# Optimization experiments

Hardware: AMD Instinct MI355X
Metric: run time of the kernel (lower is better)

Reference implementation:

```python
import jax, jax.numpy as jnp
import numpy as np

N_NODES = 100000
N_EDGES = 1600000
F_IN = 256
HID = 256
N_CLS = 16
NUM_PROP = 3


def setup_inputs() -> dict:
    key = jax.random.key(0)
    ks = jax.random.split(key, 8)
    x = jax.random.normal(ks[0], (N_NODES, F_IN), dtype=jnp.float32)
    edge_index = jax.random.randint(ks[1], (2, N_EDGES), 0, N_NODES, dtype=jnp.int64)
    # Glorot-ish scaled weights
    W1 = jax.random.normal(ks[2], (F_IN, HID), dtype=jnp.float32) / np.sqrt(F_IN)
    b1 = jnp.zeros((HID,), dtype=jnp.float32)
    Wi = jax.random.normal(ks[3], (HID, HID), dtype=jnp.float32) / np.sqrt(HID)
    bi = jnp.zeros((HID,), dtype=jnp.float32)
    W2 = jax.random.normal(ks[4], (HID, N_CLS), dtype=jnp.float32) / np.sqrt(HID)
    b2 = jnp.zeros((N_CLS,), dtype=jnp.float32)
    return {"x": x, "edge_index": edge_index, "W1": W1, "b1": b1,
            "Wi": Wi, "bi": bi, "W2": W2, "b2": b2}


def _gcn_graph(edge_index, n_nodes, dtype):
    # PyG GCNConv default: add self-loops, symmetric normalization.
    loop = jnp.arange(n_nodes, dtype=edge_index.dtype)
    src = jnp.concatenate([edge_index[0], loop])  # message source (x_j)
    dst = jnp.concatenate([edge_index[1], loop])  # aggregation target
    deg = jax.ops.segment_sum(jnp.ones_like(dst, dtype=dtype), dst, num_segments=n_nodes)
    dis = jnp.where(deg > 0, jax.lax.rsqrt(jnp.maximum(deg, 1.0)), 0.0)
    norm = dis[src] * dis[dst]  # [E+N]
    return src, dst, norm


def _gcn_conv(h, W, b, src, dst, norm, n_nodes):
    h = h @ W                                   # [N, out]
    msg = h[src] * norm[:, None]                # gather + scale, [E+N, out]
    out = jax.ops.segment_sum(msg, dst, num_segments=n_nodes)
    return out + b


def reference(x, edge_index, W1, b1, Wi, bi, W2, b2):
    n = x.shape[0]
    src, dst, norm = _gcn_graph(edge_index, n, x.dtype)
    h = _gcn_conv(x, W1, b1, src, dst, norm, n)
    # dropout p=0.25 is identity in eval mode (training=False)
    for _ in range(NUM_PROP):
        h = _gcn_conv(h, Wi, bi, src, dst, norm, n)
    h = jax.nn.relu(h)
    h = _gcn_conv(h, W2, b2, src, dst, norm, n)
    return jax.nn.softmax(h, axis=0)  # Softmax(dim=0): over nodes
```

## Files before the change

### kernel.cpp

```cpp
#include <hip/hip_runtime.h>
#include <cstdint>
#include <cstddef>

#define NFEAT 256
#define NCLS  16

typedef unsigned int uint;
typedef unsigned short ushort;
typedef __attribute__((ext_vector_type(8))) short short8;
typedef __attribute__((ext_vector_type(4))) float f32x4;

__device__ inline float blo(uint u) { return __uint_as_float(u << 16); }
__device__ inline float bhi(uint u) { return __uint_as_float(u & 0xffff0000u); }
__device__ inline ushort f2bf(float f) {
    uint b = __float_as_uint(f);
    b += 0x7fffu + ((b >> 16) & 1u);
    return (ushort)(b >> 16);
}
__device__ inline uint pack2(float a, float b) {
    return (uint)f2bf(a) | ((uint)f2bf(b) << 16);
}

__global__ void k_count(const int* __restrict__ dst, int* __restrict__ counts, int E) {
    int i = blockIdx.x * 256 + threadIdx.x;
    if (i < E) atomicAdd(&counts[dst[i]], 1);
}

__global__ void k_dis(const int* __restrict__ counts, float* __restrict__ dis, int Nn) {
    int i = blockIdx.x * 256 + threadIdx.x;
    if (i < Nn) dis[i] = rsqrtf((float)(counts[i] + 1));
}

__global__ __launch_bounds__(256) void k_bsum(const int* __restrict__ counts,
                                              int* __restrict__ bsum, int Nn) {
    int t = threadIdx.x, b = blockIdx.x;
    int i = b * 256 + t;
    int v = (i < Nn) ? counts[i] : 0;
    __shared__ int ps[256];
    ps[t] = v;
    __syncthreads();
    for (int off = 128; off > 0; off >>= 1) {
        if (t < off) ps[t] += ps[t + off];
        __syncthreads();
    }
    if (t == 0) bsum[b] = ps[0];
}

__global__ __launch_bounds__(256) void k_bscan(const int* __restrict__ bsum,
                                               int* __restrict__ boff,
                                               int nb, int* __restrict__ rowptr, int Nn) {
    int t = threadIdx.x;
    int v0 = (2 * t < nb) ? bsum[2 * t] : 0;
    int v1 = (2 * t + 1 < nb) ? bsum[2 * t + 1] : 0;
    int s = v0 + v1;
    __shared__ int ps[256];
    ps[t] = s;
    __syncthreads();
    for (int off = 1; off < 256; off <<= 1) {
        int v = (t >= off) ? ps[t - off] : 0;
        __syncthreads();
        ps[t] += v;
        __syncthreads();
    }
    int ex = ps[t] - s;
    boff[2 * t] = ex;
    boff[2 * t + 1] = ex + v0;
    if (t == 255) rowptr[Nn] = ps[255];
}

__global__ __launch_bounds__(256) void k_bwrite(const int* __restrict__ counts,
                                                const int* __restrict__ boff,
                                                int* __restrict__ rowptr,
                                                int* __restrict__ cursor, int Nn) {
    int t = threadIdx.x, b = blockIdx.x;
    int i = b * 256 + t;
    int v = (i < Nn) ? counts[i] : 0;
    __shared__ int ps[256];
    ps[t] = v;
    __syncthreads();
    for (int off = 1; off < 256; off <<= 1) {
        int u = (t >= off) ? ps[t - off] : 0;
        __syncthreads();
        ps[t] += u;
        __syncthreads();
    }
    int ex = ps[t] - v + boff[b];
    if (i < Nn) {
        rowptr[i] = ex;
        cursor[i] = ex;
    }
}

__global__ void k_fill(const int* __restrict__ src, const int* __restrict__ dst,
                       const float* __restrict__ dis, int* __restrict__ cursor,
                       int* __restrict__ csr_col, float* __restrict__ csr_val, int E) {
    int i = blockIdx.x * 256 + threadIdx.x;
    if (i < E) {
        int s = src[i], d = dst[i];
        int pos = atomicAdd(&cursor[d], 1);
        csr_col[pos] = s;
        csr_val[pos] = dis[s];
    }
}

__global__ __launch_bounds__(256) void k_mm256(const float* __restrict__ A,
                                               const float* __restrict__ B,
                                               float* __restrict__ C) {
    int i = blockIdx.x, j = threadIdx.x;
    float acc = 0.f;
    for (int k = 0; k < 256; ++k) acc = fmaf(A[i * 256 + k], B[k * 256 + j], acc);
    C[i * 256 + j] = acc;
}

__global__ __launch_bounds__(256) void k_vm256(const float* __restrict__ v,
                                               const float* __restrict__ M,
                                               float* __restrict__ r) {
    int j = threadIdx.x;
    float acc = 0.f;
    for (int k = 0; k < 256; ++k) acc = fmaf(v[k], M[(size_t)k * 256 + j], acc);
    r[j] = acc;
}

__global__ __launch_bounds__(256) void k_pack(const float* __restrict__ W,
                                              uint* __restrict__ Wp) {
    int idx = blockIdx.x * 256 + threadIdx.x;
    int w = idx & 3, lane = (idx >> 2) & 63, kstep = (idx >> 8) & 7, n16 = idx >> 11;
    int n = n16 * 16 + (lane & 15);
    int k = kstep * 32 + (lane >> 4) * 8 + 2 * w;
    Wp[idx] = pack2(W[k * 256 + n], W[(k + 1) * 256 + n]);
}

__global__ __launch_bounds__(256) void gemm_mfma(const float* __restrict__ A,
                                                 const uint* __restrict__ Wp,
                                                 ushort* __restrict__ C, int M) {
    int t = threadIdx.x;
    int wv = t >> 6;
    int l = t & 63;
    int m16 = l & 15;
    int kc = l >> 4;
    int bm = blockIdx.x * 64 + wv * 16;
    int bn = blockIdx.y * 64;
    int row = bm + m16;
    bool valid = row < M;
    const float* ap = A + (size_t)(valid ? row : 0) * 256 + kc * 8;
    const short8* wp = (const short8*)Wp;
    int n16b = bn >> 4;

    f32x4 acc0 = {0.f, 0.f, 0.f, 0.f};
    f32x4 acc1 = acc0, acc2 = acc0, acc3 = acc0;

#pragma unroll
    for (int ks = 0; ks < 8; ++ks) {
        float4 fa0 = make_float4(0.f, 0.f, 0.f, 0.f), fa1 = fa0;
        if (valid) {
            fa0 = *(const float4*)(ap + ks * 32);
            fa1 = *(const float4*)(ap + ks * 32 + 4);
        }
        short8 a;
        a[0] = (short)f2bf(fa0.x); a[1] = (short)f2bf(fa0.y);
        a[2] = (short)f2bf(fa0.z); a[3] = (short)f2bf(fa0.w);
        a[4] = (short)f2bf(fa1.x); a[5] = (short)f2bf(fa1.y);
        a[6] = (short)f2bf(fa1.z); a[7] = (short)f2bf(fa1.w);
        short8 b0 = wp[((n16b + 0) * 8 + ks) * 64 + l];
        short8 b1 = wp[((n16b + 1) * 8 + ks) * 64 + l];
        short8 b2 = wp[((n16b + 2) * 8 + ks) * 64 + l];
        short8 b3 = wp[((n16b + 3) * 8 + ks) * 64 + l];
        acc0 = __builtin_amdgcn_mfma_f32_16x16x32_bf16(a, b0, acc0, 0, 0, 0);
        acc1 = __builtin_amdgcn_mfma_f32_16x16x32_bf16(a, b1, acc1, 0, 0, 0);
        acc2 = __builtin_amdgcn_mfma_f32_16x16x32_bf16(a, b2, acc2, 0, 0, 0);
        acc3 = __builtin_amdgcn_mfma_f32_16x16x32_bf16(a, b3, acc3, 0, 0, 0);
    }

#pragma unroll
    for (int r = 0; r < 4; ++r) {
        int orow = bm + kc * 4 + r;
        if (orow < M) {
            ushort* cp = C + (size_t)orow * 256 + bn + m16;
            cp[0]  = f2bf(acc0[r]);
            cp[16] = f2bf(acc1[r]);
            cp[32] = f2bf(acc2[r]);
            cp[48] = f2bf(acc3[r]);
        }
    }
}

template <int FIRST>
__global__ __launch_bounds__(256) void k_svec(const float* __restrict__ sin,
                                              const int* __restrict__ rowptr,
                                              const int* __restrict__ col,
                                              const float* __restrict__ val,
                                              const float* __restrict__ dis,
                                              float* __restrict__ sout, int Nn) {
    int d = blockIdx.x * 256 + threadIdx.x;
    if (d >= Nn) return;
    int beg = rowptr[d], end = rowptr[d + 1];
    float acc = 0.f;
    if (FIRST) {
        for (int e = beg; e < end; ++e) acc += val[e];
    } else {
        for (int e = beg; e < end; ++e) acc = fmaf(val[e], sin[col[e]], acc);
    }
    float dd = dis[d];
    sout[d] = fmaf(dd, acc, dd * dd * (FIRST ? 1.f : sin[d]));
}

template <int FINAL>
__global__ __launch_bounds__(64) void k_aggb(const uint* __restrict__ y,
                                             const int* __restrict__ rowptr,
                                             const int* __restrict__ col,
                                             const float* __restrict__ val,
                                             const float* __restrict__ dis,
                                             const float* __restrict__ s1,
                                             const float* __restrict__ s2,
                                             const float* __restrict__ s3,
                                             const float* __restrict__ c1,
                                             const float* __restrict__ c2,
                                             const float* __restrict__ c3,
                                             const float* __restrict__ c4,
                                             uint* __restrict__ out) {
    int d = blockIdx.x;
    int t = threadIdx.x;
    const uint* yt = y + 2 * t;
    int beg = rowptr[d], end = rowptr[d + 1];
    float a0 = 0.f, a1 = 0.f, a2 = 0.f, a3 = 0.f;
    int e = beg;
    for (; e + 3 < end; e += 4) {
        int   cA = col[e],     cB = col[e + 1], cC = col[e + 2], cD = col[e + 3];
        float vA = val[e],     vB = val[e + 1], vC = val[e + 2], vD = val[e + 3];
        uint2 uA = *(const uint2*)(yt + (size_t)cA * 128);
        uint2 uB = *(const uint2*)(yt + (size_t)cB * 128);
        uint2 uC = *(const uint2*)(yt + (size_t)cC * 128);
        uint2 uD = *(const uint2*)(yt + (size_t)cD * 128);
        a0 = fmaf(vA, blo(uA.x), a0); a1 = fmaf(vA, bhi(uA.x), a1);
        a2 = fmaf(vA, blo(uA.y), a2); a3 = fmaf(vA, bhi(uA.y), a3);
        a0 = fmaf(vB, blo(uB.x), a0); a1 = fmaf(vB, bhi(uB.x), a1);
        a2 = fmaf(vB, blo(uB.y), a2); a3 = fmaf(vB, bhi(uB.y), a3);
        a0 = fmaf(vC, blo(uC.x), a0); a1 = fmaf(vC, bhi(uC.x), a1);
        a2 = fmaf(vC, blo(uC.y), a2); a3 = fmaf(vC, bhi(uC.y), a3);
        a0 = fmaf(vD, blo(uD.x), a0); a1 = fmaf(vD, bhi(uD.x), a1);
        a2 = fmaf(vD, blo(uD.y), a2); a3 = fmaf(vD, bhi(uD.y), a3);
    }
    for (; e < end; ++e) {
        int c = col[e]; float v = val[e];
        uint2 u = *(const uint2*)(yt + (size_t)c * 128);
        a0 = fmaf(v, blo(u.x), a0); a1 = fmaf(v, bhi(u.x), a1);
        a2 = fmaf(v, blo(u.y), a2); a3 = fmaf(v, bhi(u.y), a3);
    }
    float dd = dis[d];
    float d2 = dd * dd;
    uint2 us = *(const uint2*)(yt + (size_t)d * 128);
    float r0 = fmaf(dd, a0, d2 * blo(us.x));
    float r1 = fmaf(dd, a1, d2 * bhi(us.x));
    float r2 = fmaf(dd, a2, d2 * blo(us.y));
    float r3 = fmaf(dd, a3, d2 * bhi(us.y));
    if (FINAL) {
        float4 C1 = *(const float4*)(c1 + 4 * t);
        float4 C2 = *(const float4*)(c2 + 4 * t);
        float4 C3 = *(const float4*)(c3 + 4 * t);
        float4 C4 = *(const float4*)(c4 + 4 * t);
        float S1 = s1[d], S2 = s2[d], S3 = s3[d];
        r0 += S3 * C1.x + S2 * C2.x + S1 * C3.x + C4.x;
        r1 += S3 * C1.y + S2 * C2.y + S1 * C3.y + C4.y;
        r2 += S3 * C1.z + S2 * C2.z + S1 * C3.z + C4.z;
        r3 += S3 * C1.w + S2 * C2.w + S1 * C3.w + C4.w;
    }
    uint2 o;
    o.x = pack2(r0, r1);
    o.y = pack2(r2, r3);
    *(uint2*)(out + (size_t)d * 128 + 2 * t) = o;
}

__global__ __launch_bounds__(256) void k_gemm16b(const uint* __restrict__ A,
                                                 const float* __restrict__ W2,
                                                 float* __restrict__ Y, int M) {
    __shared__ float Ws[256][16];
    int t = threadIdx.x;
    for (int i = t; i < 256 * 16; i += 256) Ws[i >> 4][i & 15] = W2[i];
    __syncthreads();
    int tx = t & 15, ty = t >> 4;
    int r = blockIdx.x * 16 + ty;
    if (r >= M) return;
    const uint* a = A + (size_t)r * 128;
    float acc = 0.f;
    for (int i = 0; i < 128; i += 4) {
        uint4 u = *(const uint4*)(a + i);
        float f;
        f = fmaxf(blo(u.x), 0.f); acc = fmaf(f, Ws[2 * i + 0][tx], acc);
        f = fmaxf(bhi(u.x), 0.f); acc = fmaf(f, Ws[2 * i + 1][tx], acc);
        f = fmaxf(blo(u.y), 0.f); acc = fmaf(f, Ws[2 * i + 2][tx], acc);
        f = fmaxf(bhi(u.y), 0.f); acc = fmaf(f, Ws[2 * i + 3][tx], acc);
        f = fmaxf(blo(u.z), 0.f); acc = fmaf(f, Ws[2 * i + 4][tx], acc);
        f = fmaxf(bhi(u.z), 0.f); acc = fmaf(f, Ws[2 * i + 5][tx], acc);
        f = fmaxf(blo(u.w), 0.f); acc = fmaf(f, Ws[2 * i + 6][tx], acc);
        f = fmaxf(bhi(u.w), 0.f); acc = fmaf(f, Ws[2 * i + 7][tx], acc);
    }
    Y[(size_t)r * NCLS + tx] = acc;
}

__global__ __launch_bounds__(256) void k_agg16(const float* __restrict__ y16,
                                               const int* __restrict__ rowptr,
                                               const int* __restrict__ col,
                                               const float* __restrict__ val,
                                               const float* __restrict__ dis,
                                               const float* __restrict__ b2,
                                               float* __restrict__ out, int Nn) {
    int t = threadIdx.x;
    int tx = t & 15, ty = t >> 4;
    int d = blockIdx.x * 16 + ty;
    if (d >= Nn) return;
    int beg = rowptr[d], end = rowptr[d + 1];
    float acc = 0.f;
    for (int e = beg; e < end; ++e)
        acc = fmaf(val[e], y16[(size_t)col[e] * NCLS + tx], acc);
    float dd = dis[d];
    out[(size_t)d * NCLS + tx] = dd * acc + dd * dd * y16[(size_t)d * NCLS + tx] + b2[tx];
}

__global__ __launch_bounds__(256) void k_sm1(const float* __restrict__ z,
                                             float* __restrict__ pmax,
                                             float* __restrict__ psum, int Nn) {
    int b = blockIdx.x, t = threadIdx.x, tx = t & 15, ty = t >> 4;
    int CH = (Nn + 255) / 256;
    int r0 = b * CH, r1 = min(r0 + CH, Nn);
    __shared__ float red[16][17];
    __shared__ float gloc[16];
    float m = -3.4e38f;
    for (int r = r0 + ty; r < r1; r += 16) m = fmaxf(m, z[(size_t)r * NCLS + tx]);
    red[ty][tx] = m;
    __syncthreads();
    if (ty == 0) {
        float mm = red[0][tx];
#pragma unroll
        for (int i = 1; i < 16; ++i) mm = fmaxf(mm, red[i][tx]);
        gloc[tx] = mm;
    }
    __syncthreads();
    float g = gloc[tx];
    float s = 0.f;
    for (int r = r0 + ty; r < r1; r += 16) s += expf(z[(size_t)r * NCLS + tx] - g);
    red[ty][tx] = s;
    __syncthreads();
    if (ty == 0) {
        float ss = red[0][tx];
#pragma unroll
        for (int i = 1; i < 16; ++i) ss += red[i][tx];
        pmax[b * 16 + tx] = g;
        psum[b * 16 + tx] = ss;
    }
}

__global__ __launch_bounds__(256) void k_sm2(const float* __restrict__ pmax,
                                             const float* __restrict__ psum,
                                             float* __restrict__ g16,
                                             float* __restrict__ inv16) {
    int t = threadIdx.x, tx = t & 15, ty = t >> 4;
    __shared__ float red[16][17];
    __shared__ float gsh[16];
    float m = -3.4e38f;
    for (int b = ty; b < 256; b += 16) m = fmaxf(m, pmax[b * 16 + tx]);
    red[ty][tx] = m;
    __syncthreads();
    if (ty == 0) {
        float mm = red[0][tx];
#pragma unroll
        for (int i = 1; i < 16; ++i) mm = fmaxf(mm, red[i][tx]);
        gsh[tx] = mm;
    }
    __syncthreads();
    float g = gsh[tx];
    float s = 0.f;
    for (int b = ty; b < 256; b += 16)
        s += psum[b * 16 + tx] * expf(pmax[b * 16 + tx] - g);
    red[ty][tx] = s;
    __syncthreads();
    if (ty == 0) {
        float ss = red[0][tx];
#pragma unroll
        for (int i = 1; i < 16; ++i) ss += red[i][tx];
        g16[tx] = g;
        inv16[tx] = 1.0f / ss;
    }
}

__global__ void k_sm5(float* __restrict__ z, const float* __restrict__ g16,
                      const float* __restrict__ inv16, int total) {
    int i = blockIdx.x * 256 + threadIdx.x;
    if (i < total) {
        int c = i & 15;
        z[i] = expf(z[i] - g16[c]) * inv16[c];
    }
}

extern "C" void kernel_launch(void* const* d_in, const int* in_sizes, int n_in,
                              void* d_out, int out_size, void* d_ws, size_t ws_size,
                              hipStream_t stream) {
    const float* x  = (const float*)d_in[0];
    const int*   ei = (const int*)d_in[1];
    const float* W1 = (const float*)d_in[2];
    const float* b1 = (const float*)d_in[3];
    const float* Wi = (const float*)d_in[4];
    const float* bi = (const float*)d_in[5];
    const float* W2 = (const float*)d_in[6];
    const float* b2 = (const float*)d_in[7];
    float* out = (float*)d_out;

    int Nn = in_sizes[0] / NFEAT;
    int E  = in_sizes[1] / 2;
    const int* esrc = ei;
    const int* edst = ei + E;

    char* p = (char*)d_ws;
    auto carve = [&](size_t bytes) -> char* {
        char* r = p;
        p += (bytes + 255) / 256 * 256;
        return r;
    };
    uint*  bufA    = (uint*) carve((size_t)Nn * 128 * 4);
    uint*  bufB    = (uint*) carve((size_t)Nn * 128 * 4);
    int*   counts  = (int*)  carve((size_t)Nn * 4);
    int*   cursor  = (int*)  carve((size_t)Nn * 4);
    int*   rowptr  = (int*)  carve((size_t)(Nn + 1) * 4);
    float* dis     = (float*)carve((size_t)Nn * 4);
    int*   csr_col = (int*)  carve((size_t)E * 4);
    float* csr_val = (float*)carve((size_t)E * 4);
    float* y16     = (float*)carve((size_t)Nn * NCLS * 4);
    float* s1      = (float*)carve((size_t)Nn * 4);
    float* s2      = (float*)carve((size_t)Nn * 4);
    float* s3      = (float*)carve((size_t)Nn * 4);
    float* WA      = (float*)carve(256 * 256 * 4);
    float* WB      = (float*)carve(256 * 256 * 4);
    float* Wc      = (float*)carve(256 * 256 * 4);
    uint*  Wp      = (uint*) carve(32768 * 4);
    float* c1      = (float*)carve(256 * 4);
    float* c2      = (float*)carve(256 * 4);
    float* c3      = (float*)carve(256 * 4);
    float* u1      = (float*)carve(256 * 4);
    float* u2      = (float*)carve(256 * 4);
    int*   bsum    = (int*)  carve(512 * 4);
    int*   boff    = (int*)  carve(512 * 4);
    float* pmax    = (float*)carve(256 * 16 * 4);
    float* psum    = (float*)carve(256 * 16 * 4);
    float* g16     = (float*)carve(16 * 4);
    float* inv16   = (float*)carve(16 * 4);

    hipMemsetAsync(counts, 0, (size_t)Nn * 4, stream);

    int gE = (E + 255) / 256;
    int gN = (Nn + 255) / 256;
    k_count<<<gE, 256, 0, stream>>>(edst, counts, E);
    k_dis<<<gN, 256, 0, stream>>>(counts, dis, Nn);
    k_bsum<<<gN, 256, 0, stream>>>(counts, bsum, Nn);
    k_bscan<<<1, 256, 0, stream>>>(bsum, boff, gN, rowptr, Nn);
    k_bwrite<<<gN, 256, 0, stream>>>(counts, boff, rowptr, cursor, Nn);
    k_fill<<<gE, 256, 0, stream>>>(esrc, edst, dis, cursor, csr_col, csr_val, E);

    k_mm256<<<256, 256, 0, stream>>>(W1, Wi, WA);
    k_mm256<<<256, 256, 0, stream>>>(WA, Wi, WB);
    k_mm256<<<256, 256, 0, stream>>>(WB, Wi, Wc);
    k_pack<<<128, 256, 0, stream>>>(Wc, Wp);
    k_vm256<<<1, 256, 0, stream>>>(bi, Wi, c3);
    k_vm256<<<1, 256, 0, stream>>>(c3, Wi, c2);
    k_vm256<<<1, 256, 0, stream>>>(b1, Wi, u1);
    k_vm256<<<1, 256, 0, stream>>>(u1, Wi, u2);
    k_vm256<<<1, 256, 0, stream>>>(u2, Wi, c1);

    k_svec<1><<<gN, 256, 0, stream>>>(nullptr, rowptr, csr_col, csr_val, dis, s1, Nn);
    k_svec<0><<<gN, 256, 0, stream>>>(s1, rowptr, csr_col, csr_val, dis, s2, Nn);
    k_svec<0><<<gN, 256, 0, stream>>>(s2, rowptr, csr_col, csr_val, dis, s3, Nn);

    dim3 gg((Nn + 63) / 64, 4);
    gemm_mfma<<<gg, 256, 0, stream>>>(x, Wp, (ushort*)bufB, Nn);

    k_aggb<0><<<Nn, 64, 0, stream>>>(bufB, rowptr, csr_col, csr_val, dis,
                                     nullptr, nullptr, nullptr, nullptr, nullptr, nullptr, nullptr, bufA);
    k_aggb<0><<<Nn, 64, 0, stream>>>(bufA, rowptr, csr_col, csr_val, dis,
                                     nullptr, nullptr, nullptr, nullptr, nullptr, nullptr, nullptr, bufB);
    k_aggb<0><<<Nn, 64, 0, stream>>>(bufB, rowptr, csr_col, csr_val, dis,
                                     nullptr, nullptr, nullptr, nullptr, nullptr, nullptr, nullptr, bufA);
    k_aggb<1><<<Nn, 64, 0, stream>>>(bufA, rowptr, csr_col, csr_val, dis,
                                     s1, s2, s3, c1, c2, c3, bi, bufB);

    int g16b = (Nn + 15) / 16;
    k_gemm16b<<<g16b, 256, 0, stream>>>(bufB, W2, y16, Nn);
    k_agg16<<<g16b, 256, 0, stream>>>(y16, rowptr, csr_col, csr_val, dis, b2, out, Nn);

    k_sm1<<<256, 256, 0, stream>>>(out, pmax, psum, Nn);
    k_sm2<<<1, 256, 0, stream>>>(pmax, psum, g16, inv16);
    k_sm5<<<(Nn * NCLS + 255) / 256, 256, 0, stream>>>(out, g16, inv16, Nn * NCLS);
}
```

Baseline: 980.4 us.

## Drop CSR value array and split each wave across two edges with 16-byte gathers

Removes the csr_val array and looks up dis[col] at use time in fill, svec, aggb and agg16, which cuts the per-edge value writes and reads. The aggregation kernel now has each half-wave process alternating edges with uint4 (16-byte) row loads covering the full 256-feature bf16 row. The two halves are combined with a cross-lane shuffle. This widens memory transactions and doubles edges in flight per wave. The cost is an extra dependent random gather of dis per edge, and half the lanes sit idle in the epilogue.

```diff
diff --git a/kernel.cpp b/kernel.cpp
--- a/kernel.cpp
+++ b/kernel.cpp
@@ -92,14 +92,12 @@
 }
 
 __global__ void k_fill(const int* __restrict__ src, const int* __restrict__ dst,
-                       const float* __restrict__ dis, int* __restrict__ cursor,
-                       int* __restrict__ csr_col, float* __restrict__ csr_val, int E) {
+                       int* __restrict__ cursor, int* __restrict__ csr_col, int E) {
     int i = blockIdx.x * 256 + threadIdx.x;
     if (i < E) {
         int s = src[i], d = dst[i];
         int pos = atomicAdd(&cursor[d], 1);
         csr_col[pos] = s;
-        csr_val[pos] = dis[s];
     }
 }
 
@@ -188,7 +186,6 @@
 __global__ __launch_bounds__(256) void k_svec(const float* __restrict__ sin,
                                               const int* __restrict__ rowptr,
                                               const int* __restrict__ col,
-                                              const float* __restrict__ val,
                                               const float* __restrict__ dis,
                                               float* __restrict__ sout, int Nn) {
     int d = blockIdx.x * 256 + threadIdx.x;
@@ -196,9 +193,12 @@
     int beg = rowptr[d], end = rowptr[d + 1];
     float acc = 0.f;
     if (FIRST) {
-        for (int e = beg; e < end; ++e) acc += val[e];
+        for (int e = beg; e < end; ++e) acc += dis[col[e]];
     } else {
-        for (int e = beg; e < end; ++e) acc = fmaf(val[e], sin[col[e]], acc);
+        for (int e = beg; e < end; ++e) {
+            int c = col[e];
+            acc = fmaf(dis[c], sin[c], acc);
+        }
     }
     float dd = dis[d];
     sout[d] = fmaf(dd, acc, dd * dd * (FIRST ? 1.f : sin[d]));
@@ -208,7 +208,6 @@
 __global__ __launch_bounds__(64) void k_aggb(const uint* __restrict__ y,
                                              const int* __restrict__ rowptr,
                                              const int* __restrict__ col,
-                                             const float* __restrict__ val,
                                              const float* __restrict__ dis,
                                              const float* __restrict__ s1,
                                              const float* __restrict__ s2,
@@ -219,55 +218,88 @@
                                              const float* __restrict__ c4,
                                              uint* __restrict__ out) {
     int d = blockIdx.x;
-    int t = threadIdx.x;
-    const uint* yt = y + 2 * t;
+    int l = threadIdx.x;
+    int half = l >> 5;
+    int q = l & 31;
+    const uint4* yq = (const uint4*)y + q;
     int beg = rowptr[d], end = rowptr[d + 1];
+
     float a0 = 0.f, a1 = 0.f, a2 = 0.f, a3 = 0.f;
-    int e = beg;
-    for (; e + 3 < end; e += 4) {
-        int   cA = col[e],     cB = col[e + 1], cC = col[e + 2], cD = col[e + 3];
-        float vA = val[e],     vB = val[e + 1], vC = val[e + 2], vD = val[e + 3];
-        uint2 uA = *(const uint2*)(yt + (size_t)cA * 128);
-        uint2 uB = *(const uint2*)(yt + (size_t)cB * 128);
-        uint2 uC = *(const uint2*)(yt + (size_t)cC * 128);
-        uint2 uD = *(const uint2*)(yt + (size_t)cD * 128);
+    float a4 = 0.f, a5 = 0.f, a6 = 0.f, a7 = 0.f;
+
+    int e = beg + half;
+    for (; e + 6 < end; e += 8) {
+        int cA = col[e], cB = col[e + 2], cC = col[e + 4], cD = col[e + 6];
+        float vA = dis[cA], vB = dis[cB], vC = dis[cC], vD = dis[cD];
+        uint4 uA = yq[(size_t)cA * 32];
+        uint4 uB = yq[(size_t)cB * 32];
+        uint4 uC = yq[(size_t)cC * 32];
+        uint4 uD = yq[(size_t)cD * 32];
         a0 = fmaf(vA, blo(uA.x), a0); a1 = fmaf(vA, bhi(uA.x), a1);
         a2 = fmaf(vA, blo(uA.y), a2); a3 = fmaf(vA, bhi(uA.y), a3);
+        a4 = fmaf(vA, blo(uA.z), a4); a5 = fmaf(vA, bhi(uA.z), a5);
+        a6 = fmaf(vA, blo(uA.w), a6); a7 = fmaf(vA, bhi(uA.w), a7);
         a0 = fmaf(vB, blo(uB.x), a0); a1 = fmaf(vB, bhi(uB.x), a1);
         a2 = fmaf(vB, blo(uB.y), a2); a3 = fmaf(vB, bhi(uB.y), a3);
+        a4 = fmaf(vB, blo(uB.z), a4); a5 = fmaf(vB, bhi(uB.z), a5);
+        a6 = fmaf(vB, blo(uB.w), a6); a7 = fmaf(vB, bhi(uB.w), a7);
         a0 = fmaf(vC, blo(uC.x), a0); a1 = fmaf(vC, bhi(uC.x), a1);
         a2 = fmaf(vC, blo(uC.y), a2); a3 = fmaf(vC, bhi(uC.y), a3);
+        a4 = fmaf(vC, blo(uC.z), a4); a5 = fmaf(vC, bhi(uC.z), a5);
+        a6 = fmaf(vC, blo(uC.w), a6); a7 = fmaf(vC, bhi(uC.w), a7);
         a0 = fmaf(vD, blo(uD.x), a0); a1 = fmaf(vD, bhi(uD.x), a1);
         a2 = fmaf(vD, blo(uD.y), a2); a3 = fmaf(vD, bhi(uD.y), a3);
-    }
-    for (; e < end; ++e) {
-        int c = col[e]; float v = val[e];
-        uint2 u = *(const uint2*)(yt + (size_t)c * 128);
+        a4 = fmaf(vD, blo(uD.z), a4); a5 = fmaf(vD, bhi(uD.z), a5);
+        a6 = fmaf(vD, blo(uD.w), a6); a7 = fmaf(vD, bhi(uD.w), a7);
+    }
+    for (; e < end; e += 2) {
+        int c = col[e]; float v = dis[c];
+        uint4 u = yq[(size_t)c * 32];
         a0 = fmaf(v, blo(u.x), a0); a1 = fmaf(v, bhi(u.x), a1);
         a2 = fmaf(v, blo(u.y), a2); a3 = fmaf(v, bhi(u.y), a3);
-    }
+        a4 = fmaf(v, blo(u.z), a4); a5 = fmaf(v, bhi(u.z), a5);
+        a6 = fmaf(v, blo(u.w), a6); a7 = fmaf(v, bhi(u.w), a7);
+    }
+    a0 += __shfl_xor(a0, 32); a1 += __shfl_xor(a1, 32);
+    a2 += __shfl_xor(a2, 32); a3 += __shfl_xor(a3, 32);
+    a4 += __shfl_xor(a4, 32); a5 += __shfl_xor(a5, 32);
+    a6 += __shfl_xor(a6, 32); a7 += __shfl_xor(a7, 32);
+
+    if (half != 0) return;
+
     float dd = dis[d];
     float d2 = dd * dd;
-    uint2 us = *(const uint2*)(yt + (size_t)d * 128);
+    uint4 us = yq[(size_t)d * 32];
     float r0 = fmaf(dd, a0, d2 * blo(us.x));
     float r1 = fmaf(dd, a1, d2 * bhi(us.x));
     float r2 = fmaf(dd, a2, d2 * blo(us.y));
     float r3 = fmaf(dd, a3, d2 * bhi(us.y));
+    float r4 = fmaf(dd, a4, d2 * blo(us.z));
+    float r5 = fmaf(dd, a5, d2 * bhi(us.z));
+    float r6 = fmaf(dd, a6, d2 * blo(us.w));
+    float r7 = fmaf(dd, a7, d2 * bhi(us.w));
     if (FINAL) {
-        float4 C1 = *(const float4*)(c1 + 4 * t);
-        float4 C2 = *(const float4*)(c2 + 4 * t);
-        float4 C3 = *(const float4*)(c3 + 4 * t);
-        float4 C4 = *(const float4*)(c4 + 4 * t);
+        int fb = q * 8;
+        float4 C1a = *(const float4*)(c1 + fb), C1b = *(const float4*)(c1 + fb + 4);
+        float4 C2a = *(const float4*)(c2 + fb), C2b = *(const float4*)(c2 + fb + 4);
+        float4 C3a = *(const float4*)(c3 + fb), C3b = *(const float4*)(c3 + fb + 4);
+        float4 C4a = *(const float4*)(c4 + fb), C4b = *(const float4*)(c4 + fb + 4);
         float S1 = s1[d], S2 = s2[d], S3 = s3[d];
-        r0 += S3 * C1.x + S2 * C2.x + S1 * C3.x + C4.x;
-        r1 += S3 * C1.y + S2 * C2.y + S1 * C3.y + C4.y;
-        r2 += S3 * C1.z + S2 * C2.z + S1 * C3.z + C4.z;
-        r3 += S3 * C1.w + S2 * C2.w + S1 * C3.w + C4.w;
-    }
-    uint2 o;
+        r0 += S3 * C1a.x + S2 * C2a.x + S1 * C3a.x + C4a.x;
+        r1 += S3 * C1a.y + S2 * C2a.y + S1 * C3a.y + C4a.y;
+        r2 += S3 * C1a.z + S2 * C2a.z + S1 * C3a.z + C4a.z;
+        r3 += S3 * C1a.w + S2 * C2a.w + S1 * C3a.w + C4a.w;
+        r4 += S3 * C1b.x + S2 * C2b.x + S1 * C3b.x + C4b.x;
+        r5 += S3 * C1b.y + S2 * C2b.y + S1 * C3b.y + C4b.y;
+        r6 += S3 * C1b.z + S2 * C2b.z + S1 * C3b.z + C4b.z;
+        r7 += S3 * C1b.w + S2 * C2b.w + S1 * C3b.w + C4b.w;
+    }
+    uint4 o;
     o.x = pack2(r0, r1);
     o.y = pack2(r2, r3);
-    *(uint2*)(out + (size_t)d * 128 + 2 * t) = o;
+    o.z = pack2(r4, r5);
+    o.w = pack2(r6, r7);
+    ((uint4*)out)[(size_t)d * 32 + q] = o;
 }
 
 __global__ __launch_bounds__(256) void k_gemm16b(const uint* __restrict__ A,
@@ -300,7 +332,6 @@
 __global__ __launch_bounds__(256) void k_agg16(const float* __restrict__ y16,
                                                const int* __restrict__ rowptr,
                                                const int* __restrict__ col,
-                                               const float* __restrict__ val,
                                                const float* __restrict__ dis,
                                                const float* __restrict__ b2,
                                                float* __restrict__ out, int Nn) {
@@ -310,8 +341,10 @@
     if (d >= Nn) return;
     int beg = rowptr[d], end = rowptr[d + 1];
     float acc = 0.f;
-    for (int e = beg; e < end; ++e)
-        acc = fmaf(val[e], y16[(size_t)col[e] * NCLS + tx], acc);
+    for (int e = beg; e < end; ++e) {
+        int c = col[e];
+        acc = fmaf(dis[c], y16[(size_t)c * NCLS + tx], acc);
+    }
     float dd = dis[d];
     out[(size_t)d * NCLS + tx] = dd * acc + dd * dd * y16[(size_t)d * NCLS + tx] + b2[tx];
 }
@@ -422,7 +455,6 @@
     int*   rowptr  = (int*)  carve((size_t)(Nn + 1) * 4);
     float* dis     = (float*)carve((size_t)Nn * 4);
     int*   csr_col = (int*)  carve((size_t)E * 4);
-    float* csr_val = (float*)carve((size_t)E * 4);
     float* y16     = (float*)carve((size_t)Nn * NCLS * 4);
     float* s1      = (float*)carve((size_t)Nn * 4);
     float* s2      = (float*)carve((size_t)Nn * 4);
@@ -452,7 +484,7 @@
     k_bsum<<<gN, 256, 0, stream>>>(counts, bsum, Nn);
     k_bscan<<<1, 256, 0, stream>>>(bsum, boff, gN, rowptr, Nn);
     k_bwrite<<<gN, 256, 0, stream>>>(counts, boff, rowptr, cursor, Nn);
-    k_fill<<<gE, 256, 0, stream>>>(esrc, edst, dis, cursor, csr_col, csr_val, E);
+    k_fill<<<gE, 256, 0, stream>>>(esrc, edst, cursor, csr_col, E);
 
     k_mm256<<<256, 256, 0, stream>>>(W1, Wi, WA);
     k_mm256<<<256, 256, 0, stream>>>(WA, Wi, WB);
@@ -464,25 +496,25 @@
     k_vm256<<<1, 256, 0, stream>>>(u1, Wi, u2);
     k_vm256<<<1, 256, 0, stream>>>(u2, Wi, c1);
 
-    k_svec<1><<<gN, 256, 0, stream>>>(nullptr, rowptr, csr_col, csr_val, dis, s1, Nn);
-    k_svec<0><<<gN, 256, 0, stream>>>(s1, rowptr, csr_col, csr_val, dis, s2, Nn);
-    k_svec<0><<<gN, 256, 0, stream>>>(s2, rowptr, csr_col, csr_val, dis, s3, Nn);
+    k_svec<1><<<gN, 256, 0, stream>>>(nullptr, rowptr, csr_col, dis, s1, Nn);
+    k_svec<0><<<gN, 256, 0, stream>>>(s1, rowptr, csr_col, dis, s2, Nn);
+    k_svec<0><<<gN, 256, 0, stream>>>(s2, rowptr, csr_col, dis, s3, Nn);
 
     dim3 gg((Nn + 63) / 64, 4);
     gemm_mfma<<<gg, 256, 0, stream>>>(x, Wp, (ushort*)bufB, Nn);
 
-    k_aggb<0><<<Nn, 64, 0, stream>>>(bufB, rowptr, csr_col, csr_val, dis,
+    k_aggb<0><<<Nn, 64, 0, stream>>>(bufB, rowptr, csr_col, dis,
                                      nullptr, nullptr, nullptr, nullptr, nullptr, nullptr, nullptr, bufA);
-    k_aggb<0><<<Nn, 64, 0, stream>>>(bufA, rowptr, csr_col, csr_val, dis,
+    k_aggb<0><<<Nn, 64, 0, stream>>>(bufA, rowptr, csr_col, dis,
                                      nullptr, nullptr, nullptr, nullptr, nullptr, nullptr, nullptr, bufB);
-    k_aggb<0><<<Nn, 64, 0, stream>>>(bufB, rowptr, csr_col, csr_val, dis,
+    k_aggb<0><<<Nn, 64, 0, stream>>>(bufB, rowptr, csr_col, dis,
                                      nullptr, nullptr, nullptr, nullptr, nullptr, nullptr, nullptr, bufA);
-    k_aggb<1><<<Nn, 64, 0, stream>>>(bufA, rowptr, csr_col, csr_val, dis,
+    k_aggb<1><<<Nn, 64, 0, stream>>>(bufA, rowptr, csr_col, dis,
                                      s1, s2, s3, c1, c2, c3, bi, bufB);
 
     int g16b = (Nn + 15) / 16;
     k_gemm16b<<<g16b, 256, 0, stream>>>(bufB, W2, y16, Nn);
-    k_agg16<<<g16b, 256, 0, stream>>>(y16, rowptr, csr_col, csr_val, dis, b2, out, Nn);
+    k_agg16<<<g16b, 256, 0, stream>>>(y16, rowptr, csr_col, dis, b2, out, Nn);
 
     k_sm1<<<256, 256, 0, stream>>>(out, pmax, psum, Nn);
     k_sm2<<<1, 256, 0, stream>>>(pmax, psum, g16, inv16);
```

Result: slower. 1.025 ms (+4.6%).

## Build CSR via two-level bucketed counting sort instead of global atomics

Applied to the files above, without the earlier changes.

Replaces the per-node global atomic count and scatter with a two-pass bucket sort. Edges are first binned by destination in blocks of 256 nodes, using shared-memory histograms and a chunked local scatter into a staging buffer. A per-bucket kernel then builds row pointers, degrees and column indices with shared-memory atomics. The aim is to cut contended global atomics and random scattered writes during graph preprocessing, at the cost of an extra 8-byte-per-edge buffer, another pass over the edges, and a bucket table that assumes at most about 400 buckets in shared memory.

```diff
diff --git a/kernel.cpp b/kernel.cpp
--- a/kernel.cpp
+++ b/kernel.cpp
@@ -21,37 +21,28 @@
     return (uint)f2bf(a) | ((uint)f2bf(b) << 16);
 }
 
-__global__ void k_count(const int* __restrict__ dst, int* __restrict__ counts, int E) {
-    int i = blockIdx.x * 256 + threadIdx.x;
-    if (i < E) atomicAdd(&counts[dst[i]], 1);
-}
-
-__global__ void k_dis(const int* __restrict__ counts, float* __restrict__ dis, int Nn) {
-    int i = blockIdx.x * 256 + threadIdx.x;
-    if (i < Nn) dis[i] = rsqrtf((float)(counts[i] + 1));
-}
-
-__global__ __launch_bounds__(256) void k_bsum(const int* __restrict__ counts,
-                                              int* __restrict__ bsum, int Nn) {
-    int t = threadIdx.x, b = blockIdx.x;
-    int i = b * 256 + t;
-    int v = (i < Nn) ? counts[i] : 0;
-    __shared__ int ps[256];
-    ps[t] = v;
-    __syncthreads();
-    for (int off = 128; off > 0; off >>= 1) {
-        if (t < off) ps[t] += ps[t + off];
-        __syncthreads();
-    }
-    if (t == 0) bsum[b] = ps[0];
-}
-
-__global__ __launch_bounds__(256) void k_bscan(const int* __restrict__ bsum,
+
+__global__ __launch_bounds__(256) void k_ccount(const int* __restrict__ dst,
+                                                int* __restrict__ bhist, int E, int nb) {
+    __shared__ int h[512];
+    int t = threadIdx.x;
+    for (int i = t; i < nb; i += 256) h[i] = 0;
+    __syncthreads();
+    for (int i = blockIdx.x * 256 + t; i < E; i += gridDim.x * 256)
+        atomicAdd(&h[dst[i] >> 8], 1);
+    __syncthreads();
+    for (int i = t; i < nb; i += 256)
+        if (h[i]) atomicAdd(&bhist[i], h[i]);
+}
+
+__global__ __launch_bounds__(256) void k_cscan(const int* __restrict__ bhist,
                                                int* __restrict__ boff,
-                                               int nb, int* __restrict__ rowptr, int Nn) {
-    int t = threadIdx.x;
-    int v0 = (2 * t < nb) ? bsum[2 * t] : 0;
-    int v1 = (2 * t + 1 < nb) ? bsum[2 * t + 1] : 0;
+                                               int* __restrict__ gcur,
+                                               int* __restrict__ rowptr,
+                                               int nb, int Nn) {
+    int t = threadIdx.x;
+    int v0 = (2 * t < nb) ? bhist[2 * t] : 0;
+    int v1 = (2 * t + 1 < nb) ? bhist[2 * t + 1] : 0;
     int s = v0 + v1;
     __shared__ int ps[256];
     ps[t] = s;
@@ -63,19 +54,82 @@
         __syncthreads();
     }
     int ex = ps[t] - s;
-    boff[2 * t] = ex;
-    boff[2 * t + 1] = ex + v0;
-    if (t == 255) rowptr[Nn] = ps[255];
-}
-
-__global__ __launch_bounds__(256) void k_bwrite(const int* __restrict__ counts,
-                                                const int* __restrict__ boff,
-                                                int* __restrict__ rowptr,
-                                                int* __restrict__ cursor, int Nn) {
-    int t = threadIdx.x, b = blockIdx.x;
-    int i = b * 256 + t;
-    int v = (i < Nn) ? counts[i] : 0;
+    if (2 * t < nb)     { boff[2 * t] = ex;          gcur[2 * t] = ex; }
+    if (2 * t + 1 < nb) { boff[2 * t + 1] = ex + v0; gcur[2 * t + 1] = ex + v0; }
+    if (t == 255) { boff[nb] = ps[255]; rowptr[Nn] = ps[255]; }
+}
+
+__global__ __launch_bounds__(256) void k_cfill(const int* __restrict__ src,
+                                               const int* __restrict__ dst,
+                                               int* __restrict__ gcur,
+                                               uint2* __restrict__ ebuf, int E, int nb) {
+    __shared__ int hist[400];
+    __shared__ int lstart[400];
+    __shared__ int gbase[400];
+    __shared__ int cur[400];
     __shared__ int ps[256];
+    __shared__ uint2 stg[4096];
+    __shared__ ushort sb[4096];
+    int t = threadIdx.x;
+    int base = blockIdx.x * 4096;
+    int lim = min(4096, E - base);
+    for (int i = t; i < nb; i += 256) hist[i] = 0;
+    __syncthreads();
+    for (int k = t; k < lim; k += 256) atomicAdd(&hist[dst[base + k] >> 8], 1);
+    __syncthreads();
+    int v0 = (2 * t < nb) ? hist[2 * t] : 0;
+    int v1 = (2 * t + 1 < nb) ? hist[2 * t + 1] : 0;
+    int s = v0 + v1;
+    ps[t] = s;
+    __syncthreads();
+    for (int off = 1; off < 256; off <<= 1) {
+        int v = (t >= off) ? ps[t - off] : 0;
+        __syncthreads();
+        ps[t] += v;
+        __syncthreads();
+    }
+    int ex = ps[t] - s;
+    if (2 * t < nb) {
+        lstart[2 * t] = ex; cur[2 * t] = ex;
+        if (v0) gbase[2 * t] = atomicAdd(&gcur[2 * t], v0);
+    }
+    if (2 * t + 1 < nb) {
+        lstart[2 * t + 1] = ex + v0; cur[2 * t + 1] = ex + v0;
+        if (v1) gbase[2 * t + 1] = atomicAdd(&gcur[2 * t + 1], v1);
+    }
+    __syncthreads();
+    for (int k = t; k < lim; k += 256) {
+        int s_ = src[base + k], d_ = dst[base + k];
+        int b = d_ >> 8;
+        int slot = atomicAdd(&cur[b], 1);
+        stg[slot] = make_uint2((uint)s_, (uint)d_);
+        sb[slot] = (ushort)b;
+    }
+    __syncthreads();
+    for (int j = t; j < lim; j += 256) {
+        int b = sb[j];
+        ebuf[gbase[b] + (j - lstart[b])] = stg[j];
+    }
+}
+
+__global__ __launch_bounds__(256) void k_rowbuild(const uint2* __restrict__ ebuf,
+                                                  const int* __restrict__ boff,
+                                                  int* __restrict__ rowptr,
+                                                  float* __restrict__ dis,
+                                                  int* __restrict__ csr_col,
+                                                  int Nn, int nb) {
+    int b = blockIdx.x;
+    int t = threadIdx.x;
+    int beg = boff[b], end = boff[b + 1];
+    __shared__ int rcnt[256];
+    __shared__ int rstart[256];
+    __shared__ int ps[256];
+    rcnt[t] = 0;
+    __syncthreads();
+    for (int e = beg + t; e < end; e += 256)
+        atomicAdd(&rcnt[ebuf[e].y & 255], 1);
+    __syncthreads();
+    int v = rcnt[t];
     ps[t] = v;
     __syncthreads();
     for (int off = 1; off < 256; off <<= 1) {
@@ -84,23 +138,28 @@
         ps[t] += u;
         __syncthreads();
     }
-    int ex = ps[t] - v + boff[b];
-    if (i < Nn) {
-        rowptr[i] = ex;
-        cursor[i] = ex;
-    }
-}
-
-__global__ void k_fill(const int* __restrict__ src, const int* __restrict__ dst,
-                       const float* __restrict__ dis, int* __restrict__ cursor,
-                       int* __restrict__ csr_col, float* __restrict__ csr_val, int E) {
+    int ex = ps[t] - v;
+    int node = b * 256 + t;
+    if (node < Nn) {
+        rowptr[node] = beg + ex;
+        dis[node] = rsqrtf((float)(v + 1));
+    }
+    rstart[t] = beg + ex;
+    __syncthreads();
+    rcnt[t] = 0;
+    __syncthreads();
+    for (int e = beg + t; e < end; e += 256) {
+        uint2 ed = ebuf[e];
+        int r = ed.y & 255;
+        int slot = atomicAdd(&rcnt[r], 1);
+        csr_col[rstart[r] + slot] = (int)ed.x;
+    }
+}
+
+__global__ void k_val(const int* __restrict__ col, const float* __restrict__ dis,
+                      float* __restrict__ val, int E) {
     int i = blockIdx.x * 256 + threadIdx.x;
-    if (i < E) {
-        int s = src[i], d = dst[i];
-        int pos = atomicAdd(&cursor[d], 1);
-        csr_col[pos] = s;
-        csr_val[pos] = dis[s];
-    }
+    if (i < E) val[i] = dis[col[i]];
 }
 
 __global__ __launch_bounds__(256) void k_mm256(const float* __restrict__ A,
@@ -406,6 +465,7 @@
 
     int Nn = in_sizes[0] / NFEAT;
     int E  = in_sizes[1] / 2;
+    int nb = (Nn + 255) >> 8;
     const int* esrc = ei;
     const int* edst = ei + E;
 
@@ -417,12 +477,14 @@
     };
     uint*  bufA    = (uint*) carve((size_t)Nn * 128 * 4);
     uint*  bufB    = (uint*) carve((size_t)Nn * 128 * 4);
-    int*   counts  = (int*)  carve((size_t)Nn * 4);
-    int*   cursor  = (int*)  carve((size_t)Nn * 4);
     int*   rowptr  = (int*)  carve((size_t)(Nn + 1) * 4);
     float* dis     = (float*)carve((size_t)Nn * 4);
     int*   csr_col = (int*)  carve((size_t)E * 4);
     float* csr_val = (float*)carve((size_t)E * 4);
+    uint2* ebuf    = (uint2*)carve((size_t)E * 8);
+    int*   bhist   = (int*)  carve(512 * 4);
+    int*   boff    = (int*)  carve(512 * 4);
+    int*   gcur    = (int*)  carve(512 * 4);
     float* y16     = (float*)carve((size_t)Nn * NCLS * 4);
     float* s1      = (float*)carve((size_t)Nn * 4);
     float* s2      = (float*)carve((size_t)Nn * 4);
@@ -436,23 +498,22 @@
     float* c3      = (float*)carve(256 * 4);
     float* u1      = (float*)carve(256 * 4);
     float* u2      = (float*)carve(256 * 4);
-    int*   bsum    = (int*)  carve(512 * 4);
-    int*   boff    = (int*)  carve(512 * 4);
     float* pmax    = (float*)carve(256 * 16 * 4);
     float* psum    = (float*)carve(256 * 16 * 4);
     float* g16     = (float*)carve(16 * 4);
     float* inv16   = (float*)carve(16 * 4);
 
-    hipMemsetAsync(counts, 0, (size_t)Nn * 4, stream);
+    hipMemsetAsync(bhist, 0, 512 * 4, stream);
 
     int gE = (E + 255) / 256;
     int gN = (Nn + 255) / 256;
-    k_count<<<gE, 256, 0, stream>>>(edst, counts, E);
-    k_dis<<<gN, 256, 0, stream>>>(counts, dis, Nn);
-    k_bsum<<<gN, 256, 0, stream>>>(counts, bsum, Nn);
-    k_bscan<<<1, 256, 0, stream>>>(bsum, boff, gN, rowptr, Nn);
-    k_bwrite<<<gN, 256, 0, stream>>>(counts, boff, rowptr, cursor, Nn);
-    k_fill<<<gE, 256, 0, stream>>>(esrc, edst, dis, cursor, csr_col, csr_val, E);
+    int nch = (E + 4095) / 4096;
+
+    k_ccount<<<1024, 256, 0, stream>>>(edst, bhist, E, nb);
+    k_cscan<<<1, 256, 0, stream>>>(bhist, boff, gcur, rowptr, nb, Nn);
+    k_cfill<<<nch, 256, 0, stream>>>(esrc, edst, gcur, ebuf, E, nb);
+    k_rowbuild<<<nb, 256, 0, stream>>>(ebuf, boff, rowptr, dis, csr_col, Nn, nb);
+    k_val<<<gE, 256, 0, stream>>>(csr_col, dis, csr_val, E);
 
     k_mm256<<<256, 256, 0, stream>>>(W1, Wi, WA);
     k_mm256<<<256, 256, 0, stream>>>(WA, Wi, WB);
```

Result: faster. 902.5 us (-7.9%).
